# Performance work log

Measured on AMD Instinct MI355X. Metric: run time of the kernel, lower is better.

Reference implementation:

```python
import jax, jax.numpy as jnp
import numpy as np

B, S, M, D, DI, H, DH, DFF = 2, 1024, 1024, 1024, 1024, 16, 64, 4096
NEG = -1e30


def _ln(x, g, b, eps=1e-5):
    mu = jnp.mean(x, -1, keepdims=True)
    var = jnp.mean((x - mu) ** 2, -1, keepdims=True)
    return (x - mu) / jnp.sqrt(var + eps) * g + b


def _rel_shift(x):
    # x: (b, i, j, h) -- Transformer-XL shift via pad + reshape (exact torch trick)
    b, i, j, h = x.shape
    zp = jnp.zeros((b, 1, j, h), x.dtype)
    xp = jnp.concatenate([zp, x], axis=1).reshape(i + 1, b, j, h)
    return xp[1:].reshape(b, i, j, h)


def setup_inputs() -> dict:
    key = jax.random.key(0)
    ks = jax.random.split(key, 24)
    rn = lambda k, sh, s=1.0: jax.random.normal(k, sh, jnp.float32) * s
    St = S + M
    causal = jnp.arange(St)[None, :] > (jnp.arange(S)[:, None] + M)  # (S, St)
    tgt_mask = jnp.broadcast_to(causal[None, :, :, None], (B, S, St, 1))
    return {
        "x": rn(ks[0], (B, S, D)),
        "enc_output": rn(ks[1], (B, S, D)),
        "pos_emb": rn(ks[2], (St, DI)),
        "u": rn(ks[3], (H, DH), 0.02),
        "v": rn(ks[4], (H, DH), 0.02),
        "mem": rn(ks[5], (B, M, D)),
        "tgt_mask": tgt_mask,
        "Wq_m": rn(ks[6], (D, DI), 0.02),
        "Wkv_m": rn(ks[7], (D, 2 * DI), 0.02),
        "fcw_m": rn(ks[8], (DI, D), 0.02),
        "fcb_m": jnp.zeros((D,), jnp.float32),
        "lnm_g": jnp.ones((D,), jnp.float32),
        "lnm_b": jnp.zeros((D,), jnp.float32),
        "Wq_c": rn(ks[9], (D, DI), 0.02),
        "Wkv_c": rn(ks[10], (D, 2 * DI), 0.02),
        "fcw_c": rn(ks[11], (DI, D), 0.02),
        "fcb_c": jnp.zeros((D,), jnp.float32),
        "lnc_g": jnp.ones((D,), jnp.float32),
        "lnc_b": jnp.zeros((D,), jnp.float32),
        "W1": rn(ks[12], (D, DFF), 0.02),
        "b1": jnp.zeros((DFF,), jnp.float32),
        "W2": rn(ks[13], (DFF, D), 0.02),
        "b2": jnp.zeros((D,), jnp.float32),
        "ln1_g": jnp.ones((D,), jnp.float32),
        "ln1_b": jnp.zeros((D,), jnp.float32),
        "ln2_g": jnp.ones((D,), jnp.float32),
        "ln2_b": jnp.zeros((D,), jnp.float32),
        "ln3_g": jnp.ones((D,), jnp.float32),
        "ln3_b": jnp.zeros((D,), jnp.float32),
    }


def reference(x, enc_output, pos_emb, u, v, mem, tgt_mask,
              Wq_m, Wkv_m, fcw_m, fcb_m, lnm_g, lnm_b,
              Wq_c, Wkv_c, fcw_c, fcb_c, lnc_g, lnc_b,
              W1, b1, W2, b2,
              ln1_g, ln1_b, ln2_g, ln2_b, ln3_g, ln3_b):
    scale = 1.0 / (DH ** 0.5)

    def mha(xn):  # RecurrenceAttention (internal post-norm, pre_norm=False)
        h = jnp.concatenate([mem, xn], axis=1)                       # (B, M+S, D)
        q = (xn @ Wq_m).reshape(B, S, H, DH)
        k, vv = jnp.split(h @ Wkv_m, 2, axis=-1)
        k = k.reshape(B, S + M, H, DH)
        vv = vv.reshape(B, S + M, H, DH)
        content = jnp.einsum('bihd,bjhd->bijh', q + u, k)
        pe = pos_emb.reshape(S + M, H, DH)
        pos = jnp.einsum('bihd,jhd->bijh', q + v, pe)
        attn = content + _rel_shift(pos)
        attn = jnp.where(tgt_mask, NEG, attn)
        attn = attn * scale
        attn = jax.nn.softmax(attn, axis=1)                          # NOTE: query axis (faithful)
        o = jnp.einsum('bijh,bjhd->bihd', attn, vv).reshape(B, S, DI)
        return _ln(xn + o @ fcw_m + fcb_m, lnm_g, lnm_b)

    def cross(dec):  # CrossAttention (internal post-norm)
        q = (dec @ Wq_c).reshape(B, S, H, DH)
        k, vv = jnp.split(enc_output @ Wkv_c, 2, axis=-1)
        k = k.reshape(B, S, H, DH)
        vv = vv.reshape(B, S, H, DH)
        attn = jnp.einsum('bihd,bjhd->bijh', q, k) * scale
        attn = jax.nn.softmax(attn, axis=1)                          # query axis (faithful)
        o = jnp.einsum('bijh,bjhd->bihd', attn, vv).reshape(B, S, DI)
        return _ln(dec + o @ fcw_c + fcb_c, lnc_g, lnc_b)

    # decoder layer, pre_norm=True path
    out = x + mha(_ln(x, ln1_g, ln1_b))
    out2 = out + cross(_ln(out, ln2_g, ln2_b))
    h = jax.nn.gelu(_ln(out2, ln3_g, ln3_b) @ W1 + b1, approximate=False)
    out3 = out2 + (h @ W2 + b2)
    return out3
```

## Files before the change

kernel.cpp:

```cpp
#include <hip/hip_runtime.h>

typedef unsigned short u16;
typedef __attribute__((ext_vector_type(4))) unsigned short u16x4;
typedef __attribute__((ext_vector_type(8))) unsigned short u16x8;
typedef __attribute__((ext_vector_type(8))) __bf16 bf16x8;
typedef __attribute__((ext_vector_type(4))) float f32x4;

#define DEV __device__ __forceinline__

DEV float b2f(u16 u){ union{ unsigned int i; float f; } x; x.i = ((unsigned int)u) << 16; return x.f; }
DEV u16 f2b(float f){ unsigned int x = __float_as_uint(f); return (u16)((x + 0x7fffu + ((x >> 16) & 1u)) >> 16); }

DEV void block_red2(float& s, float& q){
#pragma unroll
  for (int off = 32; off; off >>= 1){ s += __shfl_down(s, off); q += __shfl_down(q, off); }
  __shared__ float sh1[4], sh2[4];
  int lane = threadIdx.x & 63, w = threadIdx.x >> 6;
  if (lane == 0){ sh1[w] = s; sh2[w] = q; }
  __syncthreads();
  s = sh1[0] + sh1[1] + sh1[2] + sh1[3];
  q = sh2[0] + sh2[1] + sh2[2] + sh2[3];
}

template<int WM, int WN, bool OUTB>
__global__ __launch_bounds__(WM*WN*64) void gemm_bt(
    const u16* __restrict__ A, const u16* __restrict__ Bm, void* __restrict__ Cp,
    int K, int lda, int ldb, int ldc, int Hh,
    long aob, long aoh, long bob, long boh, long cob, long coh)
{
  constexpr int BM = WM*64, BN = WN*64, BK = 64, NW = WM*WN;
  __shared__ u16 At[BM*64];
  __shared__ u16 Bt[BN*64];
  int z = blockIdx.z, b_ = z / Hh, h_ = z % Hh;
  const u16* Ab = A + (long)b_*aob + (long)h_*aoh;
  const u16* Bb = Bm + (long)b_*bob + (long)h_*boh;
  long cbase = (long)b_*cob + (long)h_*coh;
  int m0 = blockIdx.y * BM, n0 = blockIdx.x * BN;
  int tid = threadIdx.x, lane = tid & 63, wv = tid >> 6;
  int wm = wv / WN, wn = wv % WN;
  f32x4 acc[4][4];
  f32x4 z4 = {0.f, 0.f, 0.f, 0.f};
#pragma unroll
  for (int a = 0; a < 4; a++)
#pragma unroll
    for (int b = 0; b < 4; b++) acc[a][b] = z4;
  int lr = lane & 15, lk8 = (lane >> 4) * 8;
  int rq = lane >> 3, cq = (lane & 7) << 3;
  for (int k0 = 0; k0 < K; k0 += BK){
    __syncthreads();
#pragma unroll
    for (int q = wv; q < BM/8; q += NW){
      const u16* g = &Ab[(long)(m0 + q*8 + rq)*lda + k0 + cq];
      __builtin_amdgcn_global_load_lds((const __attribute__((address_space(1))) void*)g,
          (__attribute__((address_space(3))) void*)&At[q*512], 16, 0, 0);
    }
#pragma unroll
    for (int q = wv; q < BN/8; q += NW){
      const u16* g = &Bb[(long)(n0 + q*8 + rq)*ldb + k0 + cq];
      __builtin_amdgcn_global_load_lds((const __attribute__((address_space(1))) void*)g,
          (__attribute__((address_space(3))) void*)&Bt[q*512], 16, 0, 0);
    }
    __syncthreads();
#pragma unroll
    for (int kk = 0; kk < BK; kk += 32){
      bf16x8 af[4], bfr[4];
#pragma unroll
      for (int mi = 0; mi < 4; mi++) af[mi]  = *(bf16x8*)&At[(wm*64 + mi*16 + lr)*64 + kk + lk8];
#pragma unroll
      for (int ni = 0; ni < 4; ni++) bfr[ni] = *(bf16x8*)&Bt[(wn*64 + ni*16 + lr)*64 + kk + lk8];
#pragma unroll
      for (int mi = 0; mi < 4; mi++)
#pragma unroll
        for (int ni = 0; ni < 4; ni++)
          acc[mi][ni] = __builtin_amdgcn_mfma_f32_16x16x32_bf16(af[mi], bfr[ni], acc[mi][ni], 0, 0, 0);
    }
  }
  int orow = (lane >> 4) * 4, ocol = lane & 15;
#pragma unroll
  for (int mi = 0; mi < 4; mi++)
#pragma unroll
    for (int ni = 0; ni < 4; ni++){
      int row = m0 + wm*64 + mi*16 + orow;
      int col = n0 + wn*64 + ni*16 + ocol;
      long cidx = cbase + (long)row*ldc + col;
#pragma unroll
      for (int r = 0; r < 4; r++){
        float vv = acc[mi][ni][r];
        if (OUTB) ((u16*)Cp)[cidx + (long)r*ldc] = f2b(vv);
        else      ((float*)Cp)[cidx + (long)r*ldc] = vv;
      }
    }
}

template<int KD, bool MASK>
__global__ __launch_bounds__(256) void attn_passA(
    const u16* __restrict__ Kp, const u16* __restrict__ Qp, float* __restrict__ mz,
    int J, int kld, int qld,
    long kob, long koh, long qob, long qoh, int H, float scale, int mztot)
{
  constexpr int KP = KD + 8;
  __shared__ u16 Kt[64*KP];
  __shared__ u16 Qt[128*KP];
  int bh = blockIdx.y, b = bh / H, h = bh % H;
  const u16* Kb = Kp + (long)b*kob + (long)h*koh;
  const u16* Qb = Qp + (long)b*qob + (long)h*qoh;
  int j0 = blockIdx.x * 64;
  int tid = threadIdx.x, lane = tid & 63, w = tid >> 6;
  int lr = lane & 15, lk8 = (lane >> 4) * 8;
  constexpr int RCH = KD / 8;
  for (int idx = tid; idx < 64*RCH; idx += 256){
    int r = idx / RCH, c = (idx % RCH) * 8;
    *(u16x8*)&Kt[r*KP + c] = *(const u16x8*)&Kb[(long)(j0 + r)*kld + c];
  }
  float m_run[4], z_run[4];
#pragma unroll
  for (int r = 0; r < 4; r++){ m_run[r] = -3.0e38f; z_run[r] = 0.f; }
  f32x4 zz = {0.f,0.f,0.f,0.f};
  for (int it = 0; it < 8; it++){
    if (MASK && (it*128 + 127 < j0 - 1024)) continue;
    __syncthreads();
    for (int idx = tid; idx < 128*RCH; idx += 256){
      int r = idx / RCH, c = (idx % RCH) * 8;
      *(u16x8*)&Qt[r*KP + c] = *(const u16x8*)&Qb[(long)(it*128 + r)*qld + c];
    }
    __syncthreads();
    f32x4 acc[8];
#pragma unroll
    for (int ni = 0; ni < 8; ni++) acc[ni] = zz;
#pragma unroll
    for (int kk = 0; kk < KD; kk += 32){
      bf16x8 af, bq[8];
      af = *(bf16x8*)&Kt[(w*16 + lr)*KP + kk + lk8];
#pragma unroll
      for (int ni = 0; ni < 8; ni++) bq[ni] = *(bf16x8*)&Qt[(ni*16 + lr)*KP + kk + lk8];
#pragma unroll
      for (int ni = 0; ni < 8; ni++)
        acc[ni] = __builtin_amdgcn_mfma_f32_16x16x32_bf16(af, bq[ni], acc[ni], 0, 0, 0);
    }
#pragma unroll
    for (int r = 0; r < 4; r++){
      int jg = j0 + w*16 + ((lane >> 4) << 2) + r;
      float sv[8]; float tm = -3.0e38f;
#pragma unroll
      for (int ni = 0; ni < 8; ni++){
        int ig = it*128 + ni*16 + (lane & 15);
        float s = acc[ni][r] * scale;
        bool val = (!MASK) || (ig >= jg - 1024);
        sv[ni] = val ? s : -3.0e38f;
        tm = fmaxf(tm, sv[ni]);
      }
#pragma unroll
      for (int off = 1; off < 16; off <<= 1) tm = fmaxf(tm, __shfl_xor(tm, off));
      float mn = fmaxf(m_run[r], tm);
      float zt = 0.f;
#pragma unroll
      for (int ni = 0; ni < 8; ni++)
        zt += (sv[ni] > -1.0e37f) ? __expf(sv[ni] - mn) : 0.f;
#pragma unroll
      for (int off = 1; off < 16; off <<= 1) zt += __shfl_xor(zt, off);
      z_run[r] = z_run[r] * __expf(m_run[r] - mn) + zt;
      m_run[r] = mn;
    }
  }
  if ((lane & 15) == 0){
#pragma unroll
    for (int r = 0; r < 4; r++){
      int jg = j0 + w*16 + ((lane >> 4) << 2) + r;
      mz[(long)bh*J + jg] = m_run[r];
      mz[(long)mztot + (long)bh*J + jg] = 1.f / z_run[r];
    }
  }
}

template<int KD, bool MASK>
__global__ __launch_bounds__(256) void attn_passB(
    const u16* __restrict__ Kp, const u16* __restrict__ Qp, const u16* __restrict__ Vtp,
    const float* __restrict__ mz, u16* __restrict__ Op,
    int J, int kld, int qld, int vld, int oldd,
    long kob, long koh, long qob, long qoh, long vob, long voh, long oob, long ooh,
    int H, float scale, int mztot)
{
  constexpr int KP = KD + 8, PSTR = 140, VSTR = 136;
  __shared__ u16 Qt[64*KP];
  __shared__ u16 PK[128*KP];
  __shared__ u16 Vtt[64*VSTR];
  u16* Kt = PK;
  u16* Pt = PK;
  int bh = blockIdx.y, b = bh / H, h = bh % H;
  const u16* Kb = Kp + (long)b*kob + (long)h*koh;
  const u16* Qb = Qp + (long)b*qob + (long)h*qoh;
  const u16* Vb = Vtp + (long)b*vob + (long)h*voh;
  u16* Ob = Op + (long)b*oob + (long)h*ooh;
  const float* mzm = mz + (long)bh*J;
  const float* mzz = mz + (long)mztot + (long)bh*J;
  int i0 = blockIdx.x * 64;
  int tid = threadIdx.x, lane = tid & 63, w = tid >> 6;
  int lr = lane & 15, lk8 = (lane >> 4) * 8;
  constexpr int RCH = KD / 8;
  for (int idx = tid; idx < 64*RCH; idx += 256){
    int r = idx / RCH, c = (idx % RCH) * 8;
    *(u16x8*)&Qt[r*KP + c] = *(const u16x8*)&Qb[(long)(i0 + r)*qld + c];
  }
  f32x4 acc_o[4];
  f32x4 zz = {0.f,0.f,0.f,0.f};
#pragma unroll
  for (int nd = 0; nd < 4; nd++) acc_o[nd] = zz;
  int JT = J >> 7;
  for (int jt = 0; jt < JT; jt++){
    if (MASK && (jt*128 > i0 + 1087)) continue;
    __syncthreads();
    for (int idx = tid; idx < 128*RCH; idx += 256){
      int r = idx / RCH, c = (idx % RCH) * 8;
      *(u16x8*)&Kt[r*KP + c] = *(const u16x8*)&Kb[(long)(jt*128 + r)*kld + c];
    }
    for (int idx = tid; idx < 64*16; idx += 256){
      int r = idx >> 4, c = (idx & 15) << 3;
      *(u16x8*)&Vtt[r*VSTR + c] = *(const u16x8*)&Vb[(long)r*vld + jt*128 + c];
    }
    __syncthreads();
    f32x4 acc[8];
#pragma unroll
    for (int ni = 0; ni < 8; ni++) acc[ni] = zz;
#pragma unroll
    for (int kk = 0; kk < KD; kk += 32){
      bf16x8 aq, bk[8];
      aq = *(bf16x8*)&Qt[(w*16 + lr)*KP + kk + lk8];
#pragma unroll
      for (int ni = 0; ni < 8; ni++) bk[ni] = *(bf16x8*)&Kt[(ni*16 + lr)*KP + kk + lk8];
#pragma unroll
      for (int ni = 0; ni < 8; ni++)
        acc[ni] = __builtin_amdgcn_mfma_f32_16x16x32_bf16(aq, bk[ni], acc[ni], 0, 0, 0);
    }
    __syncthreads();
#pragma unroll
    for (int ni = 0; ni < 8; ni++){
      int jg = jt*128 + ni*16 + (lane & 15);
      float mj = mzm[jg], zj = mzz[jg];
#pragma unroll
      for (int r = 0; r < 4; r++){
        int ig = i0 + w*16 + ((lane >> 4) << 2) + r;
        bool val = (!MASK) || (ig >= jg - 1024);
        float p = val ? __expf(acc[ni][r] * scale - mj) * zj : 0.f;
        Pt[(w*16 + ((lane >> 4) << 2) + r)*PSTR + ni*16 + (lane & 15)] = f2b(p);
      }
    }
    __syncthreads();
#pragma unroll
    for (int kk = 0; kk < 128; kk += 32){
      bf16x8 pa, vb[4];
      pa = *(bf16x8*)&Pt[(w*16 + lr)*PSTR + kk + lk8];
#pragma unroll
      for (int nd = 0; nd < 4; nd++) vb[nd] = *(bf16x8*)&Vtt[(nd*16 + lr)*VSTR + kk + lk8];
#pragma unroll
      for (int nd = 0; nd < 4; nd++)
        acc_o[nd] = __builtin_amdgcn_mfma_f32_16x16x32_bf16(pa, vb[nd], acc_o[nd], 0, 0, 0);
    }
  }
#pragma unroll
  for (int nd = 0; nd < 4; nd++)
#pragma unroll
    for (int r = 0; r < 4; r++){
      int ig = i0 + w*16 + ((lane >> 4) << 2) + r;
      int d = nd*16 + (lane & 15);
      Ob[(long)ig*oldd + d] = f2b(acc_o[nd][r]);
    }
}

__global__ __launch_bounds__(256) void transpose_k(
    const u16* __restrict__ src, u16* __restrict__ dst,
    int lds_, int ldd, int Hh, long sob, long soh, long dob, long doh)
{
  __shared__ u16 tile[64*72];
  int z = blockIdx.z, b_ = z / Hh, h_ = z % Hh;
  const u16* S_ = src + (long)b_*sob + (long)h_*soh;
  u16* D_ = dst + (long)b_*dob + (long)h_*doh;
  int r0 = blockIdx.y * 64, c0 = blockIdx.x * 64;
  int tid = threadIdx.x;
  for (int idx = tid; idx < 512; idx += 256){
    int r = idx >> 3, c = (idx & 7) << 3;
    *(u16x8*)&tile[r*72 + c] = *(const u16x8*)&S_[(long)(r0 + r)*lds_ + c0 + c];
  }
  __syncthreads();
  for (int idx = tid; idx < 512; idx += 256){
    int c = idx >> 3, r = (idx & 7) << 3;
    u16x8 v;
#pragma unroll
    for (int e = 0; e < 8; e++) v[e] = tile[(r + e)*72 + c];
    *(u16x8*)&D_[(long)(c0 + c)*ldd + r0 + r] = v;
  }
}

__global__ __launch_bounds__(256) void transpose_cvt_k(
    const float* __restrict__ src, u16* __restrict__ dst, int lds_, int ldd)
{
  __shared__ u16 tile[64*72];
  int r0 = blockIdx.y * 64, c0 = blockIdx.x * 64;
  int tid = threadIdx.x;
  for (int idx = tid; idx < 512; idx += 256){
    int r = idx >> 3, c = (idx & 7) << 3;
    const float* s = &src[(long)(r0 + r)*lds_ + c0 + c];
#pragma unroll
    for (int e = 0; e < 8; e++) tile[r*72 + c + e] = f2b(s[e]);
  }
  __syncthreads();
  for (int idx = tid; idx < 512; idx += 256){
    int c = idx >> 3, r = (idx & 7) << 3;
    u16x8 v;
#pragma unroll
    for (int e = 0; e < 8; e++) v[e] = tile[(r + e)*72 + c];
    *(u16x8*)&dst[(long)(c0 + c)*ldd + r0 + r] = v;
  }
}

__global__ __launch_bounds__(256) void cvt_k(const float* __restrict__ src, u16* __restrict__ dst)
{
  long i = ((long)blockIdx.x*256 + threadIdx.x) * 4;
  float4 v = *(const float4*)&src[i];
  u16x4 o; o[0] = f2b(v.x); o[1] = f2b(v.y); o[2] = f2b(v.z); o[3] = f2b(v.w);
  *(u16x4*)&dst[i] = o;
}

__global__ __launch_bounds__(256) void ln_k(const float* __restrict__ src, const float* __restrict__ g,
                                            const float* __restrict__ be, u16* __restrict__ out)
{
  long base = (long)blockIdx.x * 1024;
  int tid = threadIdx.x;
  const float* s = src + base + tid*4;
  float v[4] = {s[0], s[1], s[2], s[3]};
  float s1 = v[0]+v[1]+v[2]+v[3];
  float s2 = v[0]*v[0]+v[1]*v[1]+v[2]*v[2]+v[3]*v[3];
  block_red2(s1, s2);
  float mu = s1 * (1.f/1024.f);
  float var = s2 * (1.f/1024.f) - mu*mu;
  float rs = rsqrtf(var + 1e-5f);
#pragma unroll
  for (int e = 0; e < 4; e++){
    int col = tid*4 + e;
    out[base + col] = f2b((v[e]-mu)*rs*g[col] + be[col]);
  }
}

__global__ __launch_bounds__(256) void add_ln_k(const float* __restrict__ go,
    const u16* __restrict__ xn, const float* __restrict__ bias,
    const float* __restrict__ g, const float* __restrict__ be,
    const float* __restrict__ resid, float* __restrict__ outp)
{
  const long PS = 2097152;
  long base = (long)blockIdx.x * 1024;
  int tid = threadIdx.x;
  float v[4];
#pragma unroll
  for (int e = 0; e < 4; e++){
    int col = tid*4 + e;
    long idx = base + col;
    v[e] = go[idx] + go[idx + PS] + go[idx + 2*PS] + go[idx + 3*PS] + b2f(xn[idx]) + bias[col];
  }
  float s1 = v[0]+v[1]+v[2]+v[3];
  float s2 = v[0]*v[0]+v[1]*v[1]+v[2]*v[2]+v[3]*v[3];
  block_red2(s1, s2);
  float mu = s1 * (1.f/1024.f);
  float var = s2 * (1.f/1024.f) - mu*mu;
  float rs = rsqrtf(var + 1e-5f);
#pragma unroll
  for (int e = 0; e < 4; e++){
    int col = tid*4 + e;
    outp[base + col] = resid[base + col] + (v[e]-mu)*rs*g[col] + be[col];
  }
}

__global__ __launch_bounds__(256) void build_qq(const u16* __restrict__ q, const float* __restrict__ u,
                                                const float* __restrict__ v, u16* __restrict__ QQ)
{
  int bi = blockIdx.x;
  long qrow = (long)bi * 1024;
  long obase = (long)bi * 2048;
  int n = bi + 2;
  int bp = n / 1025, ip = n % 1025;
  long qsrc = ip ? ((long)(bp*1024 + ip - 1)) * 1024 : -1;
  for (int t = threadIdx.x; t < 2048; t += 256){
    int h = t >> 7, e = t & 127;
    float val;
    if (e < 64) val = b2f(q[qrow + h*64 + e]) + u[h*64 + e];
    else {
      int d = e - 64;
      val = (qsrc < 0) ? 0.f : b2f(q[qsrc + h*64 + d]) + v[h*64 + d];
    }
    QQ[obase + t] = f2b(val);
  }
}

__global__ __launch_bounds__(256) void build_bb(const u16* __restrict__ kv, const float* __restrict__ pe,
                                                u16* __restrict__ BB)
{
  int bj = blockIdx.x;
  int j = bj & 2047;
  long kvrow = (long)bj * 2048;
  long obase = (long)bj * 2048;
  for (int t = threadIdx.x; t < 2048; t += 256){
    int h = t >> 7, e = t & 127;
    u16 val = (e < 64) ? kv[kvrow + h*64 + e] : f2b(pe[(long)j*1024 + h*64 + (e - 64)]);
    BB[obase + t] = val;
  }
}

__global__ __launch_bounds__(256) void gelu_k(const float* __restrict__ f1, const float* __restrict__ b1,
                                              u16* __restrict__ h1)
{
  long i = (long)blockIdx.x*256 + threadIdx.x;
  float x = f1[i] + b1[i & 4095];
  h1[i] = f2b(0.5f * x * (1.f + erff(x * 0.70710678118654752f)));
}

__global__ __launch_bounds__(256) void final_k(const float* __restrict__ out2, const float* __restrict__ f2,
                                               const float* __restrict__ b2v, float* __restrict__ outp)
{
  const long PS = 2097152;
  long i = (long)blockIdx.x*256 + threadIdx.x;
  outp[i] = out2[i] + f2[i] + f2[i + PS] + f2[i + 2*PS] + f2[i + 3*PS] + b2v[i & 1023];
}

extern "C" void kernel_launch(void* const* d_in, const int* in_sizes, int n_in,
                              void* d_out, int out_size, void* d_ws, size_t ws_size,
                              hipStream_t stream)
{
  (void)in_sizes; (void)n_in; (void)out_size; (void)ws_size;
  const float* X    = (const float*)d_in[0];
  const float* ENC  = (const float*)d_in[1];
  const float* PE   = (const float*)d_in[2];
  const float* Uu   = (const float*)d_in[3];
  const float* Vv   = (const float*)d_in[4];
  const float* MEM  = (const float*)d_in[5];
  const float* WQM  = (const float*)d_in[7];
  const float* WKVM = (const float*)d_in[8];
  const float* FCWM = (const float*)d_in[9];
  const float* FCBM = (const float*)d_in[10];
  const float* LNMG = (const float*)d_in[11];
  const float* LNMB = (const float*)d_in[12];
  const float* WQC  = (const float*)d_in[13];
  const float* WKVC = (const float*)d_in[14];
  const float* FCWC = (const float*)d_in[15];
  const float* FCBC = (const float*)d_in[16];
  const float* LNCG = (const float*)d_in[17];
  const float* LNCB = (const float*)d_in[18];
  const float* W1   = (const float*)d_in[19];
  const float* B1   = (const float*)d_in[20];
  const float* W2   = (const float*)d_in[21];
  const float* B2   = (const float*)d_in[22];
  const float* LN1G = (const float*)d_in[23];
  const float* LN1B = (const float*)d_in[24];
  const float* LN2G = (const float*)d_in[25];
  const float* LN2B = (const float*)d_in[26];
  const float* LN3G = (const float*)d_in[27];
  const float* LN3B = (const float*)d_in[28];
  float* OUT = (float*)d_out;
  char* W = (char*)d_ws;
  const size_t MB = 1ull << 20;

  u16*   wT_a  = (u16*)(W + 0*MB);
  u16*   wT_b  = (u16*)(W + 2*MB);
  u16*   wT_c  = (u16*)(W + 6*MB);
  u16*   w1T   = (u16*)(W + 0*MB);
  u16*   xn1   = (u16*)(W + 8*MB);
  u16*   q     = (u16*)(W + 12*MB);
  u16*   o_b   = (u16*)(W + 12*MB);
  u16*   kv    = (u16*)(W + 16*MB);
  float* outb  = (float*)(W + 24*MB);
  u16*   QQ    = (u16*)(W + 32*MB);
  u16*   xn2   = (u16*)(W + 32*MB);
  u16*   qc    = (u16*)(W + 36*MB);
  u16*   BB    = (u16*)(W + 40*MB);
  u16*   kvc   = (u16*)(W + 40*MB);
  u16*   Vtc   = (u16*)(W + 48*MB);
  u16*   oc    = (u16*)(W + 52*MB);
  u16*   Vt    = (u16*)(W + 56*MB);
  u16*   w2T   = (u16*)(W + 56*MB);
  float* mzb   = (float*)(W + 64*MB);
  u16*   memb  = (u16*)(W + 68*MB);
  u16*   encb  = (u16*)(W + 68*MB);
  float* ofc   = (float*)(W + 66*MB);
  float* f1    = (float*)(W + 66*MB);
  float* f2    = (float*)(W + 66*MB);
  u16*   h1    = (u16*)(W + 98*MB);
  float* out2b = (float*)(W + 114*MB);

  transpose_cvt_k<<<dim3(16,16),256,0,stream>>>(WQM,  wT_a, 1024,1024);
  transpose_cvt_k<<<dim3(32,16),256,0,stream>>>(WKVM, wT_b, 2048,1024);
  transpose_cvt_k<<<dim3(16,16),256,0,stream>>>(FCWM, wT_c, 1024,1024);
  cvt_k<<<2048,256,0,stream>>>(MEM, memb);
  ln_k<<<2048,256,0,stream>>>(X, LN1G, LN1B, xn1);
  gemm_bt<2,2,true><<<dim3(8,16,1),256,0,stream>>>(xn1, wT_a, q, 1024, 1024,1024,1024, 1, 0,0,0,0,0,0);
  gemm_bt<2,2,true><<<dim3(16,8,2),256,0,stream>>>(memb, wT_b, kv, 1024, 1024,1024,2048, 1,
      1048576,0, 0,0, 4194304,0);
  gemm_bt<2,2,true><<<dim3(16,8,2),256,0,stream>>>(xn1, wT_b, kv + (size_t)1024*2048, 1024, 1024,1024,2048, 1,
      1048576,0, 0,0, 4194304,0);
  build_qq<<<2048,256,0,stream>>>(q, Uu, Vv, QQ);
  build_bb<<<4096,256,0,stream>>>(kv, PE, BB);
  transpose_k<<<dim3(1,32,32),256,0,stream>>>(kv + 1024, Vt, 2048, 2048, 16,
      4194304,64, 2097152,131072);
  attn_passA<128,true><<<dim3(32,32),256,0,stream>>>(BB, QQ, mzb, 2048, 2048, 2048,
      4194304,128, 2097152,128, 16, 0.125f, 65536);
  attn_passB<128,true><<<dim3(16,32),256,0,stream>>>(BB, QQ, Vt, mzb, o_b, 2048,
      2048,2048,2048,1024, 4194304,128, 2097152,128, 2097152,131072, 1048576,64, 16, 0.125f, 65536);
  gemm_bt<2,2,false><<<dim3(8,16,4),256,0,stream>>>(o_b, wT_c, ofc, 256, 1024,1024,1024, 4,
      0,256, 0,256, 0,2097152);
  add_ln_k<<<2048,256,0,stream>>>(ofc, xn1, FCBM, LNMG, LNMB, X, outb);

  transpose_cvt_k<<<dim3(16,16),256,0,stream>>>(WQC,  wT_a, 1024,1024);
  transpose_cvt_k<<<dim3(32,16),256,0,stream>>>(WKVC, wT_b, 2048,1024);
  transpose_cvt_k<<<dim3(16,16),256,0,stream>>>(FCWC, wT_c, 1024,1024);
  cvt_k<<<2048,256,0,stream>>>(ENC, encb);
  ln_k<<<2048,256,0,stream>>>(outb, LN2G, LN2B, xn2);
  gemm_bt<2,2,true><<<dim3(8,16,1),256,0,stream>>>(xn2, wT_a, qc, 1024, 1024,1024,1024, 1, 0,0,0,0,0,0);
  gemm_bt<2,2,true><<<dim3(16,16,1),256,0,stream>>>(encb, wT_b, kvc, 1024, 1024,1024,2048, 1, 0,0,0,0,0,0);
  transpose_k<<<dim3(1,16,32),256,0,stream>>>(kvc + 1024, Vtc, 2048, 1024, 16,
      2097152,64, 1048576,65536);
  attn_passA<64,false><<<dim3(16,32),256,0,stream>>>(kvc, qc, mzb, 1024, 2048, 1024,
      2097152,64, 1048576,64, 16, 0.125f, 32768);
  attn_passB<64,false><<<dim3(16,32),256,0,stream>>>(kvc, qc, Vtc, mzb, oc, 1024,
      2048,1024,1024,1024, 2097152,64, 1048576,64, 1048576,65536, 1048576,64, 16, 0.125f, 32768);
  gemm_bt<2,2,false><<<dim3(8,16,4),256,0,stream>>>(oc, wT_c, ofc, 256, 1024,1024,1024, 4,
      0,256, 0,256, 0,2097152);
  add_ln_k<<<2048,256,0,stream>>>(ofc, xn2, FCBC, LNCG, LNCB, outb, out2b);

  transpose_cvt_k<<<dim3(64,16),256,0,stream>>>(W1, w1T, 4096,1024);
  transpose_cvt_k<<<dim3(16,64),256,0,stream>>>(W2, w2T, 1024,4096);
  ln_k<<<2048,256,0,stream>>>(out2b, LN3G, LN3B, xn2);
  gemm_bt<2,2,false><<<dim3(32,16,1),256,0,stream>>>(xn2, w1T, f1, 1024, 1024,1024,4096, 1, 0,0,0,0,0,0);
  gelu_k<<<32768,256,0,stream>>>(f1, B1, h1);
  gemm_bt<2,2,false><<<dim3(8,16,4),256,0,stream>>>(h1, w2T, f2, 1024, 4096,4096,1024, 4,
      0,1024, 0,1024, 0,2097152);
  final_k<<<8192,256,0,stream>>>(out2b, f2, B2, OUT);
}
```

Baseline: 769.1 us.

## Split attention pass B over key halves and keep Q/K fragments in registers

Pass B of both attentions now splits the key/column loop into two halves along a new grid dimension. Each half writes fp32 partial outputs, and a new combine kernel sums them and converts to bf16. This doubles the number of blocks to fill more CUs, at the cost of extra global traffic and one more launch. Both passes also load the per-wave A operand (K in pass A, Q in pass B) straight into registers instead of staging it through LDS. One redundant barrier between the per-wave P write and the P read is removed.

```diff
diff --git a/kernel.cpp b/kernel.cpp
--- a/kernel.cpp
+++ b/kernel.cpp
@@ -99,7 +99,6 @@
     long kob, long koh, long qob, long qoh, int H, float scale, int mztot)
 {
   constexpr int KP = KD + 8;
-  __shared__ u16 Kt[64*KP];
   __shared__ u16 Qt[128*KP];
   int bh = blockIdx.y, b = bh / H, h = bh % H;
   const u16* Kb = Kp + (long)b*kob + (long)h*koh;
@@ -108,9 +107,11 @@
   int tid = threadIdx.x, lane = tid & 63, w = tid >> 6;
   int lr = lane & 15, lk8 = (lane >> 4) * 8;
   constexpr int RCH = KD / 8;
-  for (int idx = tid; idx < 64*RCH; idx += 256){
-    int r = idx / RCH, c = (idx % RCH) * 8;
-    *(u16x8*)&Kt[r*KP + c] = *(const u16x8*)&Kb[(long)(j0 + r)*kld + c];
+  bf16x8 ak[KD/32];
+  {
+    const u16* kr = &Kb[(long)(j0 + w*16 + lr)*kld];
+#pragma unroll
+    for (int kk = 0; kk < KD/32; kk++) ak[kk] = *(const bf16x8*)&kr[kk*32 + lk8];
   }
   float m_run[4], z_run[4];
 #pragma unroll
@@ -129,13 +130,12 @@
     for (int ni = 0; ni < 8; ni++) acc[ni] = zz;
 #pragma unroll
     for (int kk = 0; kk < KD; kk += 32){
-      bf16x8 af, bq[8];
-      af = *(bf16x8*)&Kt[(w*16 + lr)*KP + kk + lk8];
+      bf16x8 bq[8];
 #pragma unroll
       for (int ni = 0; ni < 8; ni++) bq[ni] = *(bf16x8*)&Qt[(ni*16 + lr)*KP + kk + lk8];
 #pragma unroll
       for (int ni = 0; ni < 8; ni++)
-        acc[ni] = __builtin_amdgcn_mfma_f32_16x16x32_bf16(af, bq[ni], acc[ni], 0, 0, 0);
+        acc[ni] = __builtin_amdgcn_mfma_f32_16x16x32_bf16(ak[kk/32], bq[ni], acc[ni], 0, 0, 0);
     }
 #pragma unroll
     for (int r = 0; r < 4; r++){
@@ -175,38 +175,40 @@
 template<int KD, bool MASK>
 __global__ __launch_bounds__(256) void attn_passB(
     const u16* __restrict__ Kp, const u16* __restrict__ Qp, const u16* __restrict__ Vtp,
-    const float* __restrict__ mz, u16* __restrict__ Op,
+    const float* __restrict__ mz, float* __restrict__ Op,
     int J, int kld, int qld, int vld, int oldd,
     long kob, long koh, long qob, long qoh, long vob, long voh, long oob, long ooh,
-    int H, float scale, int mztot)
+    int H, float scale, int mztot, int jtHalf, long opstride)
 {
   constexpr int KP = KD + 8, PSTR = 140, VSTR = 136;
-  __shared__ u16 Qt[64*KP];
   __shared__ u16 PK[128*KP];
   __shared__ u16 Vtt[64*VSTR];
   u16* Kt = PK;
   u16* Pt = PK;
   int bh = blockIdx.y, b = bh / H, h = bh % H;
+  int jh = blockIdx.z;
   const u16* Kb = Kp + (long)b*kob + (long)h*koh;
   const u16* Qb = Qp + (long)b*qob + (long)h*qoh;
   const u16* Vb = Vtp + (long)b*vob + (long)h*voh;
-  u16* Ob = Op + (long)b*oob + (long)h*ooh;
+  float* Ob = Op + (long)jh*opstride + (long)b*oob + (long)h*ooh;
   const float* mzm = mz + (long)bh*J;
   const float* mzz = mz + (long)mztot + (long)bh*J;
   int i0 = blockIdx.x * 64;
   int tid = threadIdx.x, lane = tid & 63, w = tid >> 6;
   int lr = lane & 15, lk8 = (lane >> 4) * 8;
   constexpr int RCH = KD / 8;
-  for (int idx = tid; idx < 64*RCH; idx += 256){
-    int r = idx / RCH, c = (idx % RCH) * 8;
-    *(u16x8*)&Qt[r*KP + c] = *(const u16x8*)&Qb[(long)(i0 + r)*qld + c];
+  bf16x8 aq[KD/32];
+  {
+    const u16* qr = &Qb[(long)(i0 + w*16 + lr)*qld];
+#pragma unroll
+    for (int kk = 0; kk < KD/32; kk++) aq[kk] = *(const bf16x8*)&qr[kk*32 + lk8];
   }
   f32x4 acc_o[4];
   f32x4 zz = {0.f,0.f,0.f,0.f};
 #pragma unroll
   for (int nd = 0; nd < 4; nd++) acc_o[nd] = zz;
-  int JT = J >> 7;
-  for (int jt = 0; jt < JT; jt++){
+  int jt1 = (jh + 1) * jtHalf;
+  for (int jt = jh * jtHalf; jt < jt1; jt++){
     if (MASK && (jt*128 > i0 + 1087)) continue;
     __syncthreads();
     for (int idx = tid; idx < 128*RCH; idx += 256){
@@ -223,13 +225,12 @@
     for (int ni = 0; ni < 8; ni++) acc[ni] = zz;
 #pragma unroll
     for (int kk = 0; kk < KD; kk += 32){
-      bf16x8 aq, bk[8];
-      aq = *(bf16x8*)&Qt[(w*16 + lr)*KP + kk + lk8];
+      bf16x8 bk[8];
 #pragma unroll
       for (int ni = 0; ni < 8; ni++) bk[ni] = *(bf16x8*)&Kt[(ni*16 + lr)*KP + kk + lk8];
 #pragma unroll
       for (int ni = 0; ni < 8; ni++)
-        acc[ni] = __builtin_amdgcn_mfma_f32_16x16x32_bf16(aq, bk[ni], acc[ni], 0, 0, 0);
+        acc[ni] = __builtin_amdgcn_mfma_f32_16x16x32_bf16(aq[kk/32], bk[ni], acc[ni], 0, 0, 0);
     }
     __syncthreads();
 #pragma unroll
@@ -244,7 +245,6 @@
         Pt[(w*16 + ((lane >> 4) << 2) + r)*PSTR + ni*16 + (lane & 15)] = f2b(p);
       }
     }
-    __syncthreads();
 #pragma unroll
     for (int kk = 0; kk < 128; kk += 32){
       bf16x8 pa, vb[4];
@@ -262,8 +262,20 @@
     for (int r = 0; r < 4; r++){
       int ig = i0 + w*16 + ((lane >> 4) << 2) + r;
       int d = nd*16 + (lane & 15);
-      Ob[(long)ig*oldd + d] = f2b(acc_o[nd][r]);
-    }
+      Ob[(long)ig*oldd + d] = acc_o[nd][r];
+    }
+}
+
+__global__ __launch_bounds__(256) void combine_o(const float* __restrict__ p, u16* __restrict__ o)
+{
+  const long PS = 2097152;
+  long i = ((long)blockIdx.x*256 + threadIdx.x) * 4;
+  const float* a = &p[i];
+  const float* b = &p[i + PS];
+  u16x4 r;
+#pragma unroll
+  for (int e = 0; e < 4; e++) r[e] = f2b(a[e] + b[e]);
+  *(u16x4*)&o[i] = r;
 }
 
 __global__ __launch_bounds__(256) void transpose_k(
@@ -477,6 +489,7 @@
   float* mzb   = (float*)(W + 64*MB);
   u16*   memb  = (u16*)(W + 68*MB);
   u16*   encb  = (u16*)(W + 68*MB);
+  float* opart = (float*)(W + 66*MB);
   float* ofc   = (float*)(W + 66*MB);
   float* f1    = (float*)(W + 66*MB);
   float* f2    = (float*)(W + 66*MB);
@@ -499,8 +512,10 @@
       4194304,64, 2097152,131072);
   attn_passA<128,true><<<dim3(32,32),256,0,stream>>>(BB, QQ, mzb, 2048, 2048, 2048,
       4194304,128, 2097152,128, 16, 0.125f, 65536);
-  attn_passB<128,true><<<dim3(16,32),256,0,stream>>>(BB, QQ, Vt, mzb, o_b, 2048,
-      2048,2048,2048,1024, 4194304,128, 2097152,128, 2097152,131072, 1048576,64, 16, 0.125f, 65536);
+  attn_passB<128,true><<<dim3(16,32,2),256,0,stream>>>(BB, QQ, Vt, mzb, opart, 2048,
+      2048,2048,2048,1024, 4194304,128, 2097152,128, 2097152,131072, 1048576,64, 16, 0.125f, 65536,
+      8, 2097152);
+  combine_o<<<2048,256,0,stream>>>(opart, o_b);
   gemm_bt<2,2,false><<<dim3(8,16,4),256,0,stream>>>(o_b, wT_c, ofc, 256, 1024,1024,1024, 4,
       0,256, 0,256, 0,2097152);
   add_ln_k<<<2048,256,0,stream>>>(ofc, xn1, FCBM, LNMG, LNMB, X, outb);
@@ -516,8 +531,10 @@
       2097152,64, 1048576,65536);
   attn_passA<64,false><<<dim3(16,32),256,0,stream>>>(kvc, qc, mzb, 1024, 2048, 1024,
       2097152,64, 1048576,64, 16, 0.125f, 32768);
-  attn_passB<64,false><<<dim3(16,32),256,0,stream>>>(kvc, qc, Vtc, mzb, oc, 1024,
-      2048,1024,1024,1024, 2097152,64, 1048576,64, 1048576,65536, 1048576,64, 16, 0.125f, 32768);
+  attn_passB<64,false><<<dim3(16,32,2),256,0,stream>>>(kvc, qc, Vtc, mzb, opart, 1024,
+      2048,1024,1024,1024, 2097152,64, 1048576,64, 1048576,65536, 1048576,64, 16, 0.125f, 32768,
+      4, 2097152);
+  combine_o<<<2048,256,0,stream>>>(opart, oc);
   gemm_bt<2,2,false><<<dim3(8,16,4),256,0,stream>>>(oc, wT_c, ofc, 256, 1024,1024,1024, 4,
       0,256, 0,256, 0,2097152);
   add_ln_k<<<2048,256,0,stream>>>(ofc, xn2, FCBC, LNCG, LNCB, outb, out2b);
```

Result: faster. 733.0 us (-4.7%).
